# Performance work log

Measured on AMD Instinct MI355X. Metric: run time of the kernel, lower is better.

The kernel has to match this reference:

```python
import jax, jax.numpy as jnp
import numpy as np

B, T, D = 4, 2048, 1024
E, K, F = 8, 2, 4096


def setup_inputs() -> dict:
    key = jax.random.key(0)
    ks = jax.random.split(key, 6)
    s = 0.02
    return {
        "x": jax.random.normal(ks[0], (B, T, D), dtype=jnp.float32),
        "gate_w": jax.random.normal(ks[1], (D, E), dtype=jnp.float32) * s,
        "w1": jax.random.normal(ks[2], (E, D, F), dtype=jnp.float32) * s,
        "b1": jax.random.normal(ks[3], (E, F), dtype=jnp.float32) * s,
        "w2": jax.random.normal(ks[4], (E, F, D), dtype=jnp.float32) * s,
        "b2": jax.random.normal(ks[5], (E, D), dtype=jnp.float32) * s,
    }


def reference(x, gate_w, w1, b1, w2, b2):
    b, t, d = x.shape
    xf = x.reshape(-1, d)                       # [N, D]
    logits = xf @ gate_w                        # [N, E]
    topv, topi = jax.lax.top_k(logits, K)       # [N, K]
    gates = jax.nn.softmax(topv, axis=-1)       # [N, K]
    # per-token per-expert combine weight (zero for unselected experts)
    onehot = jax.nn.one_hot(topi, E, dtype=xf.dtype)       # [N, K, E]
    comb = jnp.einsum('nk,nke->ne', gates, onehot)          # [N, E]
    out = jnp.zeros_like(xf)
    for e in range(E):  # small fixed expert loop; keeps [N,F] intermediate only
        h = jax.nn.gelu(xf @ w1[e] + b1[e], approximate=False)  # [N, F]
        y = h @ w2[e] + b2[e]                                   # [N, D]
        out = out + comb[:, e:e + 1] * y
    return out.reshape(b, t, d)
```

## Files before the change

kernel.cpp:

```cpp
#include <hip/hip_runtime.h>
#include <stdint.h>
#include <stddef.h>

#define N_TOK 8192
#define DIM   1024
#define NE    8
#define NF    4096
#define TM    256
#define BKK   64
#define RCAP  (N_TOK*2 + NE*TM)
#define MAXMT (N_TOK/TM)
#define KS2   2

typedef __attribute__((ext_vector_type(8))) short short8;
typedef __attribute__((ext_vector_type(4))) float f32x4;

__device__ __forceinline__ float bf2f(short s){
  unsigned u = ((unsigned)(unsigned short)s) << 16;
  return __builtin_bit_cast(float, u);
}
__device__ __forceinline__ short f2bf(float f){
  unsigned u = __builtin_bit_cast(unsigned, f);
  u += 0x7fffu + ((u >> 16) & 1u);
  return (short)(u >> 16);
}

#define GLD_LDS16(g, l) __builtin_amdgcn_global_load_lds( \
    (const __attribute__((address_space(1))) void*)(g),   \
    (__attribute__((address_space(3))) void*)(l), 16, 0, 0)

__device__ __forceinline__ void xcd_map(int nx, int& xo, int& mt, int& e){
  int h   = blockIdx.x + nx * (blockIdx.y + MAXMT * blockIdx.z);
  int nwg = nx * MAXMT * NE;
  int q   = nwg >> 3;
  int wk  = (h & 7) * q + (h >> 3);
  xo = wk % nx;
  int r = wk / nx;
  mt = r % MAXMT;
  e  = r / MAXMT;
}

__global__ __launch_bounds__(256) void gate_kernel(
    const float* __restrict__ x, const float* __restrict__ gw,
    int* __restrict__ topi, float* __restrict__ gatev, int* __restrict__ ctrl)
{
  int t = blockIdx.x * 4 + (threadIdx.x >> 6);
  int lane = threadIdx.x & 63;
  const float* xr = x + (size_t)t * DIM;
  float p[NE];
  #pragma unroll
  for (int e = 0; e < NE; e++) p[e] = 0.f;
  for (int i = lane; i < DIM; i += 64){
    float xv = xr[i];
    const float* g = gw + i * NE;
    #pragma unroll
    for (int e = 0; e < NE; e++) p[e] += xv * g[e];
  }
  #pragma unroll
  for (int off = 32; off > 0; off >>= 1){
    #pragma unroll
    for (int e = 0; e < NE; e++) p[e] += __shfl_xor(p[e], off, 64);
  }
  if (lane == 0){
    int i1 = 0; float v1 = p[0];
    #pragma unroll
    for (int e = 1; e < NE; e++) if (p[e] > v1){ v1 = p[e]; i1 = e; }
    int i2 = -1; float v2 = -3.4e38f;
    #pragma unroll
    for (int e = 0; e < NE; e++) if (e != i1 && p[e] > v2){ v2 = p[e]; i2 = e; }
    float ex = expf(v2 - v1);
    float g2 = ex / (1.f + ex);
    float g1 = 1.f - g2;
    topi[t*2]   = i1;  topi[t*2+1]  = i2;
    gatev[t*2]  = g1;  gatev[t*2+1] = g2;
    atomicAdd(&ctrl[i1], 1);
    atomicAdd(&ctrl[i2], 1);
  }
}

__global__ void scan_kernel(int* ctrl){
  if (threadIdx.x == 0){
    int tot = 0;
    for (int e = 0; e < NE; e++){
      int c = ctrl[e];
      int cap = (c + TM - 1) & ~(TM - 1);
      ctrl[16+e] = tot; ctrl[24+e] = cap; tot += cap;
    }
  }
}

__global__ __launch_bounds__(256) void scatter_kernel(
    const int* __restrict__ topi, int* ctrl,
    int* __restrict__ rowTok, int* __restrict__ tok2row)
{
  int t = blockIdx.x * 256 + threadIdx.x;
  #pragma unroll
  for (int k = 0; k < 2; k++){
    int e = topi[t*2 + k];
    int pos = atomicAdd(&ctrl[8+e], 1);
    int r = ctrl[16+e] + pos;
    rowTok[r] = t;
    tok2row[t*2 + k] = r;
  }
}

__global__ void pad_kernel(const int* __restrict__ ctrl, int* __restrict__ rowTok){
  int e = blockIdx.x;
  int cnt = ctrl[e], cap = ctrl[24+e], off = ctrl[16+e];
  for (int i = cnt + threadIdx.x; i < cap; i += blockDim.x)
    rowTok[off + i] = N_TOK;
}

__global__ __launch_bounds__(256) void cast_x_kernel(
    const float* __restrict__ x, short* __restrict__ xb)
{
  size_t i = ((size_t)blockIdx.x * 256 + threadIdx.x) * 8;
  if (i >= (size_t)(N_TOK + 1) * DIM) return;
  short8 o;
  if (i < (size_t)N_TOK * DIM){
    #pragma unroll
    for (int j = 0; j < 8; j++) o[j] = f2bf(x[i + j]);
  } else {
    #pragma unroll
    for (int j = 0; j < 8; j++) o[j] = 0;
  }
  *(short8*)(xb + i) = o;
}

__global__ __launch_bounds__(256) void transpose_cast_kernel(
    const float* __restrict__ src, short* __restrict__ dst, int Kd, int Nd)
{
  __shared__ float Ls[64][65];
  int e = blockIdx.z;
  int k0 = blockIdx.y * 64, n0 = blockIdx.x * 64;
  const float* s = src + (size_t)e * Kd * Nd;
  short*       d = dst + (size_t)e * Kd * Nd;
  int t = threadIdx.x;
  int kr = t >> 4, nc = (t & 15) * 4;
  #pragma unroll
  for (int rr = 0; rr < 4; rr++){
    int k = rr*16 + kr;
    f32x4 v = *(const f32x4*)(s + (size_t)(k0 + k) * Nd + n0 + nc);
    Ls[k][nc+0] = v[0]; Ls[k][nc+1] = v[1];
    Ls[k][nc+2] = v[2]; Ls[k][nc+3] = v[3];
  }
  __syncthreads();
  int nr = t >> 2, kc = (t & 3) * 16;
  short o[16];
  #pragma unroll
  for (int i = 0; i < 16; i++) o[i] = f2bf(Ls[kc + i][nr]);
  short* dp = d + (size_t)(n0 + nr) * Kd + k0 + kc;
  *(short8*)(dp)     = *(short8*)&o[0];
  *(short8*)(dp + 8) = *(short8*)&o[8];
}


#define FFN_DECLS                                                       \
  __shared__ __align__(16) short As[2][256][BKK];                       \
  __shared__ __align__(16) short Bs[2][256][BKK];                       \
  int tid = threadIdx.x, w = tid >> 6, lane = tid & 63;                 \
  int rsub = lane >> 3, ksub = lane & 7;                                \
  int sw = (ksub ^ rsub) * 8;                                           \
  char* const AsB = (char*)As; char* const BsB = (char*)Bs;             \
  int ml = lane & 15, q = lane >> 4;                                    \
  int wm = w >> 2, wn = w & 3;                                          \
  int mx = ml & 7;                                                      \
  f32x4 acc[8][4];                                                      \
  _Pragma("unroll")                                                     \
  for (int i = 0; i < 8; i++){                                          \
    _Pragma("unroll")                                                   \
    for (int j = 0; j < 4; j++){ f32x4 z = {0.f,0.f,0.f,0.f}; acc[i][j] = z; } \
  }

#define FFN_STAGE(kt, s) do{                                            \
    char* aB_ = AsB + (s)*32768; char* bB_ = BsB + (s)*32768;           \
    _Pragma("unroll")                                                   \
    for (int j = 0; j < 4; j++) GLD_LDS16(ap[j] + (kt)*BKK, aB_ + (w*4+j)*1024); \
    _Pragma("unroll")                                                   \
    for (int j = 0; j < 4; j++) GLD_LDS16(bp[j] + (kt)*BKK, bB_ + (w*4+j)*1024); \
  } while(0)

#define FFN_PROLOGUE                                                    \
  FFN_STAGE(0, 0);                                                      \
  FFN_STAGE(1, 1);                                                      \
  asm volatile("s_waitcnt vmcnt(8)" ::: "memory");                      \
  __builtin_amdgcn_sched_barrier(0);                                    \
  __builtin_amdgcn_s_barrier();

#define LDA(mh)                                                         \
  _Pragma("unroll")                                                     \
  for (int mi = 0; mi < 4; mi++){                                       \
    _Pragma("unroll")                                                   \
    for (int ks = 0; ks < 2; ks++)                                      \
      aq[mi][ks] = Ar[(wm*128 + (mh)*64 + mi*16 + ml)*8 + ((ks*4+q)^mx)]; \
  }

#define LDB_ALL                                                         \
  _Pragma("unroll")                                                     \
  for (int ni = 0; ni < 4; ni++){                                       \
    _Pragma("unroll")                                                   \
    for (int ks = 0; ks < 2; ks++)                                      \
      bq[ni][ks] = Br[(wn*64 + ni*16 + ml)*8 + ((ks*4+q)^mx)];          \
  }

#define MFMA_Q(mh, nh)                                                  \
  __builtin_amdgcn_s_barrier();                                         \
  __builtin_amdgcn_s_setprio(1);                                        \
  _Pragma("unroll")                                                     \
  for (int mi = 0; mi < 4; mi++){                                       \
    _Pragma("unroll")                                                   \
    for (int ni = 0; ni < 2; ni++){                                     \
      _Pragma("unroll")                                                 \
      for (int ks = 0; ks < 2; ks++)                                    \
        acc[(mh)*4+mi][(nh)*2+ni] = __builtin_amdgcn_mfma_f32_16x16x32_bf16( \
            aq[mi][ks], bq[(nh)*2+ni][ks], acc[(mh)*4+mi][(nh)*2+ni], 0, 0, 0); \
    }                                                                   \
  }                                                                     \
  __builtin_amdgcn_s_setprio(0);

#define FFN_ITER_BODY(s)                                                \
  const short8* Ar = (const short8*)(AsB + (s)*32768);                  \
  const short8* Br = (const short8*)(BsB + (s)*32768);                  \
  LDA(0); LDB_ALL;                                                      \
  MFMA_Q(0, 0);                                                         \
  MFMA_Q(0, 1);                                                         \
  LDA(1);                                                               \
  MFMA_Q(1, 0);                                                         \
  MFMA_Q(1, 1);

#define FFN_BOUNDARY(t, NT)                                             \
  __builtin_amdgcn_s_barrier();                                         \
  __builtin_amdgcn_sched_barrier(0);                                    \
  if ((t) + 2 < (NT)) { FFN_STAGE((t)+2, (t)&1); }                      \
  if ((t) + 1 < (NT)){                                                  \
    if ((t) + 2 < (NT)) { asm volatile("s_waitcnt vmcnt(8)" ::: "memory"); } \
    else                { asm volatile("s_waitcnt vmcnt(0)" ::: "memory"); } \
    __builtin_amdgcn_sched_barrier(0);                                  \
    __builtin_amdgcn_s_barrier();                                       \
  }

__global__ __launch_bounds__(512, 2) void ffn1_kernel(
    const short* __restrict__ Xb, const short* __restrict__ W1t,
    const float* __restrict__ b1, const int* __restrict__ ctrl,
    const int* __restrict__ rowTok, short* __restrict__ H)
{
  int e, mt, nb;
  xcd_map(NF/256, nb, mt, e);
  int cap = ctrl[24+e];
  if (mt * 256 >= cap) return;
  int rowbase = ctrl[16+e] + mt * 256;

  FFN_DECLS;

  const short* ap[4];
  #pragma unroll
  for (int j = 0; j < 4; j++){
    int g = rowTok[rowbase + w*32 + j*8 + rsub];
    ap[j] = Xb + (size_t)g * DIM + sw;
  }
  const short* bbase = W1t + ((size_t)e * NF + (size_t)nb * 256) * DIM;
  const short* bp[4];
  #pragma unroll
  for (int j = 0; j < 4; j++)
    bp[j] = bbase + (size_t)(w*32 + j*8 + rsub) * DIM + sw;

  FFN_PROLOGUE;

  const int NT = DIM / BKK;
  short8 aq[4][2], bq[4][2];
  for (int t = 0; t < NT; t++){
    int s = t & 1;
    { FFN_ITER_BODY(s); }
    FFN_BOUNDARY(t, NT);
  }

  #pragma unroll
  for (int ni = 0; ni < 4; ni++){
    int f = nb*256 + wn*64 + ni*16 + ml;
    float bb = b1[e*NF + f];
    #pragma unroll
    for (int mh = 0; mh < 2; mh++){
      #pragma unroll
      for (int mi = 0; mi < 4; mi++){
        #pragma unroll
        for (int r = 0; r < 4; r++){
          int m = wm*128 + mh*64 + mi*16 + q*4 + r;
          float v = acc[mh*4+mi][ni][r] + bb;
          float h = 0.5f * v * (1.f + erff(v * 0.70710678118654752f));
          H[(size_t)(rowbase + m) * NF + f] = f2bf(h);
        }
      }
    }
  }
}

__global__ __launch_bounds__(512, 2) void ffn2_kernel(
    const short* __restrict__ H, const short* __restrict__ W2t,
    const int* __restrict__ ctrl, float* __restrict__ Yf)
{
  int e, mt, xo;
  xcd_map((DIM/256)*KS2, xo, mt, e);
  int nb = xo & 3, kc = xo >> 2;
  int cap = ctrl[24+e];
  if (mt * 256 >= cap) return;
  int rowbase = ctrl[16+e] + mt * 256;

  FFN_DECLS;

  const short* ap[4];
  #pragma unroll
  for (int j = 0; j < 4; j++){
    int r = rowbase + w*32 + j*8 + rsub;
    ap[j] = H + (size_t)r * NF + (size_t)kc * (NF/KS2) + sw;
  }
  const short* bbase = W2t + ((size_t)e * DIM + (size_t)nb * 256) * NF;
  const short* bp[4];
  #pragma unroll
  for (int j = 0; j < 4; j++)
    bp[j] = bbase + (size_t)(w*32 + j*8 + rsub) * NF + (size_t)kc * (NF/KS2) + sw;

  FFN_PROLOGUE;

  const int NT = (NF/KS2) / BKK;
  short8 aq[4][2], bq[4][2];
  for (int t = 0; t < NT; t++){
    int s = t & 1;
    { FFN_ITER_BODY(s); }
    FFN_BOUNDARY(t, NT);
  }

  #pragma unroll
  for (int ni = 0; ni < 4; ni++){
    int d = nb*256 + wn*64 + ni*16 + ml;
    #pragma unroll
    for (int mh = 0; mh < 2; mh++){
      #pragma unroll
      for (int mi = 0; mi < 4; mi++){
        #pragma unroll
        for (int r = 0; r < 4; r++){
          int m = wm*128 + mh*64 + mi*16 + q*4 + r;
          atomicAdd(&Yf[(size_t)(rowbase + m) * DIM + d], acc[mh*4+mi][ni][r]);
        }
      }
    }
  }
}

__global__ __launch_bounds__(256) void combine_kernel(
    const float* __restrict__ Yf, const int* __restrict__ tok2row,
    const int* __restrict__ topi, const float* __restrict__ gatev,
    const float* __restrict__ b2, float* __restrict__ out)
{
  int idx = blockIdx.x * 256 + threadIdx.x;
  int t = idx >> 7, d8 = idx & 127;
  int r0 = tok2row[t*2], r1 = tok2row[t*2 + 1];
  int e0 = topi[t*2],    e1 = topi[t*2 + 1];
  float g0 = gatev[t*2], g1 = gatev[t*2 + 1];
  const f32x4* y0 = (const f32x4*)(Yf + (size_t)r0 * DIM + d8*8);
  const f32x4* y1 = (const f32x4*)(Yf + (size_t)r1 * DIM + d8*8);
  const f32x4* c0 = (const f32x4*)(b2 + (size_t)e0 * DIM + d8*8);
  const f32x4* c1 = (const f32x4*)(b2 + (size_t)e1 * DIM + d8*8);
  f32x4* dst = (f32x4*)(out + (size_t)t * DIM + d8*8);
  #pragma unroll
  for (int h = 0; h < 2; h++){
    f32x4 o;
    #pragma unroll
    for (int j = 0; j < 4; j++)
      o[j] = g0 * (y0[h][j] + c0[h][j]) + g1 * (y1[h][j] + c1[h][j]);
    dst[h] = o;
  }
}

extern "C" void kernel_launch(void* const* d_in, const int* in_sizes, int n_in,
                              void* d_out, int out_size, void* d_ws, size_t ws_size,
                              hipStream_t stream)
{
  const float* x  = (const float*)d_in[0];
  const float* gw = (const float*)d_in[1];
  const float* w1 = (const float*)d_in[2];
  const float* b1 = (const float*)d_in[3];
  const float* w2 = (const float*)d_in[4];
  const float* b2 = (const float*)d_in[5];
  float* out = (float*)d_out;

  char* ws = (char*)d_ws;
  size_t o = 0;
  int*   ctrl    = (int*)(ws + o); o += 256;
  int*   topi    = (int*)(ws + o); o += (size_t)N_TOK*2*4;
  float* gatev   = (float*)(ws + o); o += (size_t)N_TOK*2*4;
  int*   rowTok  = (int*)(ws + o); o += (size_t)RCAP*4;
  int*   tok2row = (int*)(ws + o); o += (size_t)N_TOK*2*4;
  o = (o + 255) & ~(size_t)255;
  short* Xb  = (short*)(ws + o); o += (size_t)(N_TOK + 1)*DIM*2;
  short* W1t = (short*)(ws + o); o += (size_t)NE*DIM*NF*2;
  short* W2t = (short*)(ws + o); o += (size_t)NE*NF*DIM*2;
  short* H   = (short*)(ws + o); o += (size_t)RCAP*NF*2;
  float* Yf  = (float*)(ws + o); o += (size_t)RCAP*DIM*4;
  (void)in_sizes; (void)n_in; (void)out_size;

  if (o > ws_size) return;

  hipMemsetAsync(ctrl, 0, 256, stream);
  hipMemsetAsync(Yf, 0, (size_t)RCAP*DIM*4, stream);
  gate_kernel<<<N_TOK/4, 256, 0, stream>>>(x, gw, topi, gatev, ctrl);
  scan_kernel<<<1, 64, 0, stream>>>(ctrl);
  scatter_kernel<<<N_TOK/256, 256, 0, stream>>>(topi, ctrl, rowTok, tok2row);
  pad_kernel<<<NE, 256, 0, stream>>>(ctrl, rowTok);
  cast_x_kernel<<<((N_TOK + 1)*DIM/8 + 255)/256, 256, 0, stream>>>(x, Xb);
  transpose_cast_kernel<<<dim3(NF/64, DIM/64, NE), 256, 0, stream>>>(w1, W1t, DIM, NF);
  transpose_cast_kernel<<<dim3(DIM/64, NF/64, NE), 256, 0, stream>>>(w2, W2t, NF, DIM);
  ffn1_kernel<<<dim3(NF/256, MAXMT, NE), 512, 0, stream>>>(Xb, W1t, b1, ctrl, rowTok, H);
  ffn2_kernel<<<dim3((DIM/256)*KS2, MAXMT, NE), 512, 0, stream>>>(H, W2t, ctrl, Yf);
  combine_kernel<<<N_TOK*(DIM/8)/256, 256, 0, stream>>>(Yf, tok2row, topi, gatev, b2, out);
}
```

Baseline: 1.239 ms.

## Interleave LDS prefetch into MFMA quarters and replace split-K atomics with bf16 partials

The GEMM main loop is restructured so the next tile's global-to-LDS loads are issued midway through the MFMA quarters rather than at a separate boundary, and the fragment loads are split into smaller register arrays. The aim is to overlap memory traffic with compute and reduce register pressure. ffn2 now writes its two split-K partials as separate bf16 buffers instead of fp32 atomicAdd into a zeroed buffer, which removes the memset and the atomic traffic. combine sums the two partials. Storing partials in bf16 adds rounding error in exchange for less memory traffic.

```diff
diff --git a/kernel.cpp b/kernel.cpp
--- a/kernel.cpp
+++ b/kernel.cpp
@@ -172,39 +172,7 @@
     for (int j = 0; j < 4; j++){ f32x4 z = {0.f,0.f,0.f,0.f}; acc[i][j] = z; } \
   }
 
-#define FFN_STAGE(kt, s) do{                                            \
-    char* aB_ = AsB + (s)*32768; char* bB_ = BsB + (s)*32768;           \
-    _Pragma("unroll")                                                   \
-    for (int j = 0; j < 4; j++) GLD_LDS16(ap[j] + (kt)*BKK, aB_ + (w*4+j)*1024); \
-    _Pragma("unroll")                                                   \
-    for (int j = 0; j < 4; j++) GLD_LDS16(bp[j] + (kt)*BKK, bB_ + (w*4+j)*1024); \
-  } while(0)
-
-#define FFN_PROLOGUE                                                    \
-  FFN_STAGE(0, 0);                                                      \
-  FFN_STAGE(1, 1);                                                      \
-  asm volatile("s_waitcnt vmcnt(8)" ::: "memory");                      \
-  __builtin_amdgcn_sched_barrier(0);                                    \
-  __builtin_amdgcn_s_barrier();
-
-#define LDA(mh)                                                         \
-  _Pragma("unroll")                                                     \
-  for (int mi = 0; mi < 4; mi++){                                       \
-    _Pragma("unroll")                                                   \
-    for (int ks = 0; ks < 2; ks++)                                      \
-      aq[mi][ks] = Ar[(wm*128 + (mh)*64 + mi*16 + ml)*8 + ((ks*4+q)^mx)]; \
-  }
-
-#define LDB_ALL                                                         \
-  _Pragma("unroll")                                                     \
-  for (int ni = 0; ni < 4; ni++){                                       \
-    _Pragma("unroll")                                                   \
-    for (int ks = 0; ks < 2; ks++)                                      \
-      bq[ni][ks] = Br[(wn*64 + ni*16 + ml)*8 + ((ks*4+q)^mx)];          \
-  }
-
-#define MFMA_Q(mh, nh)                                                  \
-  __builtin_amdgcn_s_barrier();                                         \
+#define MFMA_Q2(A_, mh, B_, nh)                                         \
   __builtin_amdgcn_s_setprio(1);                                        \
   _Pragma("unroll")                                                     \
   for (int mi = 0; mi < 4; mi++){                                       \
@@ -213,31 +181,85 @@
       _Pragma("unroll")                                                 \
       for (int ks = 0; ks < 2; ks++)                                    \
         acc[(mh)*4+mi][(nh)*2+ni] = __builtin_amdgcn_mfma_f32_16x16x32_bf16( \
-            aq[mi][ks], bq[(nh)*2+ni][ks], acc[(mh)*4+mi][(nh)*2+ni], 0, 0, 0); \
+            A_[mi][ks], B_[(nh)*2+ni][ks], acc[(mh)*4+mi][(nh)*2+ni], 0, 0, 0); \
     }                                                                   \
   }                                                                     \
   __builtin_amdgcn_s_setprio(0);
 
-#define FFN_ITER_BODY(s)                                                \
-  const short8* Ar = (const short8*)(AsB + (s)*32768);                  \
-  const short8* Br = (const short8*)(BsB + (s)*32768);                  \
-  LDA(0); LDB_ALL;                                                      \
-  MFMA_Q(0, 0);                                                         \
-  MFMA_Q(0, 1);                                                         \
-  LDA(1);                                                               \
-  MFMA_Q(1, 0);                                                         \
-  MFMA_Q(1, 1);
-
-#define FFN_BOUNDARY(t, NT)                                             \
+#define FFN_TILE(s, DO_STAGE, DO_W8, DO_W0)                             \
+  {                                                                     \
+    const short8* Ar = (const short8*)(AsB + (s)*32768);                \
+    const short8* Br = (const short8*)(BsB + (s)*32768);                \
+    short8 a[4][2], b[4][2];                                            \
+                                              \
+    _Pragma("unroll") for (int mi = 0; mi < 4; mi++)                    \
+      _Pragma("unroll") for (int ks = 0; ks < 2; ks++)                  \
+        a[mi][ks] = Ar[(wm*128 + mi*16 + ml)*8 + ((ks*4+q)^mx)];        \
+    _Pragma("unroll") for (int ni = 0; ni < 2; ni++)                    \
+      _Pragma("unroll") for (int ks = 0; ks < 2; ks++)                  \
+        b[ni][ks] = Br[(wn*64 + ni*16 + ml)*8 + ((ks*4+q)^mx)];         \
+    __builtin_amdgcn_s_barrier();                                       \
+    MFMA_Q2(a, 0, b, 0);                                                \
+    __builtin_amdgcn_s_barrier();                                       \
+                           \
+    _Pragma("unroll") for (int ni = 2; ni < 4; ni++)                    \
+      _Pragma("unroll") for (int ks = 0; ks < 2; ks++)                  \
+        b[ni][ks] = Br[(wn*64 + ni*16 + ml)*8 + ((ks*4+q)^mx)];         \
+    MFMA_Q2(a, 0, b, 1);                                                \
+    __builtin_amdgcn_s_barrier();                                       \
+     \
+     \
+    _Pragma("unroll") for (int mi = 0; mi < 4; mi++)                    \
+      _Pragma("unroll") for (int ks = 0; ks < 2; ks++)                  \
+        a[mi][ks] = Ar[(wm*128 + 64 + mi*16 + ml)*8 + ((ks*4+q)^mx)];   \
+    asm volatile("s_waitcnt lgkmcnt(0)" ::: "memory");                  \
+    __builtin_amdgcn_sched_barrier(0);                                  \
+    __builtin_amdgcn_s_barrier();                                       \
+    if (DO_STAGE){                                                      \
+      _Pragma("unroll")                                                 \
+      for (int j = 0; j < 4; j++) GLD_LDS16(apg[j], AsB + (s)*32768 + (w*4+j)*1024); \
+    }                                                                   \
+    MFMA_Q2(a, 1, b, 0);                                                \
+    __builtin_amdgcn_s_barrier();                                       \
+    if (DO_STAGE){                                                      \
+      _Pragma("unroll")                                                 \
+      for (int j = 0; j < 4; j++) GLD_LDS16(bpg[j], BsB + (s)*32768 + (w*4+j)*1024); \
+      _Pragma("unroll")                                                 \
+      for (int j = 0; j < 4; j++){ apg[j] += BKK; bpg[j] += BKK; }      \
+    }                                                                   \
+    MFMA_Q2(a, 1, b, 1);                                                \
+    if (DO_W8){ asm volatile("s_waitcnt vmcnt(8)" ::: "memory");        \
+                __builtin_amdgcn_sched_barrier(0); }                    \
+    if (DO_W0){ asm volatile("s_waitcnt vmcnt(0)" ::: "memory");        \
+                __builtin_amdgcn_sched_barrier(0); }                    \
+    __builtin_amdgcn_s_barrier();                                       \
+  }
+
+#define FFN_PROLOGUE                                                    \
+  _Pragma("unroll")                                                     \
+  for (int j = 0; j < 4; j++) GLD_LDS16(ap[j],       AsB + (w*4+j)*1024);          \
+  _Pragma("unroll")                                                     \
+  for (int j = 0; j < 4; j++) GLD_LDS16(bp[j],       BsB + (w*4+j)*1024);          \
+  _Pragma("unroll")                                                     \
+  for (int j = 0; j < 4; j++) GLD_LDS16(ap[j] + BKK, AsB + 32768 + (w*4+j)*1024);  \
+  _Pragma("unroll")                                                     \
+  for (int j = 0; j < 4; j++) GLD_LDS16(bp[j] + BKK, BsB + 32768 + (w*4+j)*1024);  \
+  asm volatile("s_waitcnt vmcnt(8)" ::: "memory");                      \
+  __builtin_amdgcn_sched_barrier(0);                                    \
   __builtin_amdgcn_s_barrier();                                         \
-  __builtin_amdgcn_sched_barrier(0);                                    \
-  if ((t) + 2 < (NT)) { FFN_STAGE((t)+2, (t)&1); }                      \
-  if ((t) + 1 < (NT)){                                                  \
-    if ((t) + 2 < (NT)) { asm volatile("s_waitcnt vmcnt(8)" ::: "memory"); } \
-    else                { asm volatile("s_waitcnt vmcnt(0)" ::: "memory"); } \
-    __builtin_amdgcn_sched_barrier(0);                                  \
-    __builtin_amdgcn_s_barrier();                                       \
-  }
+  const short* apg[4]; const short* bpg[4];                             \
+  _Pragma("unroll")                                                     \
+  for (int j = 0; j < 4; j++){ apg[j] = ap[j] + 2*BKK; bpg[j] = bp[j] + 2*BKK; }
+
+#define FFN_MAIN(NT)                                                    \
+  FFN_PROLOGUE;                                                         \
+  _Pragma("unroll 1")                                                   \
+  for (int t = 0; t < (NT) - 2; t++){                                   \
+    int s_ = t & 1;                                                     \
+    FFN_TILE(s_, 1, 1, 0);                                              \
+  }                                                                     \
+  FFN_TILE(((NT)-2) & 1, 0, 0, 1);                                      \
+  FFN_TILE(((NT)-1) & 1, 0, 0, 0);
 
 __global__ __launch_bounds__(512, 2) void ffn1_kernel(
     const short* __restrict__ Xb, const short* __restrict__ W1t,
@@ -264,15 +286,7 @@
   for (int j = 0; j < 4; j++)
     bp[j] = bbase + (size_t)(w*32 + j*8 + rsub) * DIM + sw;
 
-  FFN_PROLOGUE;
-
-  const int NT = DIM / BKK;
-  short8 aq[4][2], bq[4][2];
-  for (int t = 0; t < NT; t++){
-    int s = t & 1;
-    { FFN_ITER_BODY(s); }
-    FFN_BOUNDARY(t, NT);
-  }
+  FFN_MAIN(DIM/BKK);
 
   #pragma unroll
   for (int ni = 0; ni < 4; ni++){
@@ -296,7 +310,7 @@
 
 __global__ __launch_bounds__(512, 2) void ffn2_kernel(
     const short* __restrict__ H, const short* __restrict__ W2t,
-    const int* __restrict__ ctrl, float* __restrict__ Yf)
+    const int* __restrict__ ctrl, short* __restrict__ Yp)
 {
   int e, mt, xo;
   xcd_map((DIM/256)*KS2, xo, mt, e);
@@ -319,16 +333,9 @@
   for (int j = 0; j < 4; j++)
     bp[j] = bbase + (size_t)(w*32 + j*8 + rsub) * NF + (size_t)kc * (NF/KS2) + sw;
 
-  FFN_PROLOGUE;
-
-  const int NT = (NF/KS2) / BKK;
-  short8 aq[4][2], bq[4][2];
-  for (int t = 0; t < NT; t++){
-    int s = t & 1;
-    { FFN_ITER_BODY(s); }
-    FFN_BOUNDARY(t, NT);
-  }
-
+  FFN_MAIN((NF/KS2)/BKK);
+
+  short* Yk = Yp + (size_t)kc * RCAP * DIM;
   #pragma unroll
   for (int ni = 0; ni < 4; ni++){
     int d = nb*256 + wn*64 + ni*16 + ml;
@@ -339,7 +346,7 @@
         #pragma unroll
         for (int r = 0; r < 4; r++){
           int m = wm*128 + mh*64 + mi*16 + q*4 + r;
-          atomicAdd(&Yf[(size_t)(rowbase + m) * DIM + d], acc[mh*4+mi][ni][r]);
+          Yk[(size_t)(rowbase + m) * DIM + d] = f2bf(acc[mh*4+mi][ni][r]);
         }
       }
     }
@@ -347,7 +354,7 @@
 }
 
 __global__ __launch_bounds__(256) void combine_kernel(
-    const float* __restrict__ Yf, const int* __restrict__ tok2row,
+    const short* __restrict__ Yp, const int* __restrict__ tok2row,
     const int* __restrict__ topi, const float* __restrict__ gatev,
     const float* __restrict__ b2, float* __restrict__ out)
 {
@@ -356,19 +363,22 @@
   int r0 = tok2row[t*2], r1 = tok2row[t*2 + 1];
   int e0 = topi[t*2],    e1 = topi[t*2 + 1];
   float g0 = gatev[t*2], g1 = gatev[t*2 + 1];
-  const f32x4* y0 = (const f32x4*)(Yf + (size_t)r0 * DIM + d8*8);
-  const f32x4* y1 = (const f32x4*)(Yf + (size_t)r1 * DIM + d8*8);
-  const f32x4* c0 = (const f32x4*)(b2 + (size_t)e0 * DIM + d8*8);
-  const f32x4* c1 = (const f32x4*)(b2 + (size_t)e1 * DIM + d8*8);
+  const size_t half = (size_t)RCAP * DIM;
+  short8 y0a = *(const short8*)(Yp + (size_t)r0 * DIM + d8*8);
+  short8 y0b = *(const short8*)(Yp + half + (size_t)r0 * DIM + d8*8);
+  short8 y1a = *(const short8*)(Yp + (size_t)r1 * DIM + d8*8);
+  short8 y1b = *(const short8*)(Yp + half + (size_t)r1 * DIM + d8*8);
+  const float* c0 = b2 + (size_t)e0 * DIM + d8*8;
+  const float* c1 = b2 + (size_t)e1 * DIM + d8*8;
+  float o[8];
+  #pragma unroll
+  for (int j = 0; j < 8; j++)
+    o[j] = g0 * (bf2f(y0a[j]) + bf2f(y0b[j]) + c0[j])
+         + g1 * (bf2f(y1a[j]) + bf2f(y1b[j]) + c1[j]);
+  f32x4 v0 = {o[0], o[1], o[2], o[3]};
+  f32x4 v1 = {o[4], o[5], o[6], o[7]};
   f32x4* dst = (f32x4*)(out + (size_t)t * DIM + d8*8);
-  #pragma unroll
-  for (int h = 0; h < 2; h++){
-    f32x4 o;
-    #pragma unroll
-    for (int j = 0; j < 4; j++)
-      o[j] = g0 * (y0[h][j] + c0[h][j]) + g1 * (y1[h][j] + c1[h][j]);
-    dst[h] = o;
-  }
+  dst[0] = v0; dst[1] = v1;
 }
 
 extern "C" void kernel_launch(void* const* d_in, const int* in_sizes, int n_in,
@@ -395,13 +405,12 @@
   short* W1t = (short*)(ws + o); o += (size_t)NE*DIM*NF*2;
   short* W2t = (short*)(ws + o); o += (size_t)NE*NF*DIM*2;
   short* H   = (short*)(ws + o); o += (size_t)RCAP*NF*2;
-  float* Yf  = (float*)(ws + o); o += (size_t)RCAP*DIM*4;
+  short* Yp  = (short*)(ws + o); o += (size_t)KS2*RCAP*DIM*2;
   (void)in_sizes; (void)n_in; (void)out_size;
 
   if (o > ws_size) return;
 
   hipMemsetAsync(ctrl, 0, 256, stream);
-  hipMemsetAsync(Yf, 0, (size_t)RCAP*DIM*4, stream);
   gate_kernel<<<N_TOK/4, 256, 0, stream>>>(x, gw, topi, gatev, ctrl);
   scan_kernel<<<1, 64, 0, stream>>>(ctrl);
   scatter_kernel<<<N_TOK/256, 256, 0, stream>>>(topi, ctrl, rowTok, tok2row);
@@ -410,6 +419,6 @@
   transpose_cast_kernel<<<dim3(NF/64, DIM/64, NE), 256, 0, stream>>>(w1, W1t, DIM, NF);
   transpose_cast_kernel<<<dim3(DIM/64, NF/64, NE), 256, 0, stream>>>(w2, W2t, NF, DIM);
   ffn1_kernel<<<dim3(NF/256, MAXMT, NE), 512, 0, stream>>>(Xb, W1t, b1, ctrl, rowTok, H);
-  ffn2_kernel<<<dim3((DIM/256)*KS2, MAXMT, NE), 512, 0, stream>>>(H, W2t, ctrl, Yf);
-  combine_kernel<<<N_TOK*(DIM/8)/256, 256, 0, stream>>>(Yf, tok2row, topi, gatev, b2, out);
-}
+  ffn2_kernel<<<dim3((DIM/256)*KS2, MAXMT, NE), 512, 0, stream>>>(H, W2t, ctrl, Yp);
+  combine_kernel<<<N_TOK*(DIM/8)/256, 256, 0, stream>>>(Yp, tok2row, topi, gatev, b2, out);
+}
```

New measurement: 1.119 ms. 1.11x faster.
